# Performance work log

Hardware: AMD Instinct MI355X
Metric: run time of the kernel (lower is better)

## Reference

```python
import jax, jax.numpy as jnp
import numpy as np

HIDDEN = 2048
NUM_HEADS = 16
HEAD_DIM = HIDDEN // NUM_HEADS  # 128
SCALE = HEAD_DIM ** -0.5


def setup_inputs() -> dict:
    key = jax.random.key(0)
    ks = jax.random.split(key, 5)
    B, S = 2, 2048
    init = HIDDEN ** -0.5  # roughly kaiming-uniform scale for Linear weights
    return {
        "hidden_states": jax.random.normal(ks[0], (B, S, HIDDEN), dtype=jnp.float32),
        "Wq": jax.random.normal(ks[1], (HIDDEN, HIDDEN), dtype=jnp.float32) * init,
        "Wk": jax.random.normal(ks[2], (HIDDEN, HIDDEN), dtype=jnp.float32) * init,
        "Wv": jax.random.normal(ks[3], (HIDDEN, HIDDEN), dtype=jnp.float32) * init,
        "Wo": jax.random.normal(ks[4], (HIDDEN, HIDDEN), dtype=jnp.float32) * init,
    }


def reference(hidden_states, Wq, Wk, Wv, Wo):
    B, S, _ = hidden_states.shape
    # Projections (nn.Linear: x @ W.T; weights stored as [out, in])
    q = (hidden_states @ Wq.T).reshape(B, S, NUM_HEADS, HEAD_DIM).transpose(0, 2, 1, 3)
    k = (hidden_states @ Wk.T).reshape(B, S, NUM_HEADS, HEAD_DIM).transpose(0, 2, 1, 3)
    v = (hidden_states @ Wv.T).reshape(B, S, NUM_HEADS, HEAD_DIM).transpose(0, 2, 1, 3)
    # Full quadratic attention (faithful to the source's explicit materialization)
    scores = jnp.einsum("bhqd,bhkd->bhqk", q, k) * SCALE  # [B,H,S,S]
    probs = jax.nn.softmax(scores, axis=-1)
    attn = jnp.einsum("bhqk,bhkd->bhqd", probs, v)  # [B,H,S,Dh]
    attn = attn.transpose(0, 2, 1, 3).reshape(B, S, HIDDEN)
    return attn @ Wo.T
```

## Files before the change

kernel.cpp:

```cpp
#include <hip/hip_runtime.h>
#include <cstdint>

#define HIDDEN 2048
#define NHEADS 16
#define DH 128
#define BATCH 2
#define SEQ 2048
#define MTOT 4096
#define BH (BATCH * NHEADS)

typedef __attribute__((ext_vector_type(8))) short bf16x8;
typedef __attribute__((ext_vector_type(4))) float f32x4;

static constexpr float QSCALE = (float)(0.08838834764831845 * 1.4426950408889634);

__device__ __forceinline__ unsigned short f2bf(float f) {
  union { float f; uint32_t u; } v; v.f = f;
  uint32_t r = v.u + 0x7FFFu + ((v.u >> 16) & 1u);
  return (unsigned short)(r >> 16);
}
__device__ __forceinline__ uint32_t cvtpk(float lo, float hi) {
  uint32_t r;
  asm("v_cvt_pk_bf16_f32 %0, %1, %2" : "=v"(r) : "v"(lo), "v"(hi));
  return r;
}
__device__ __forceinline__ f32x4 mfma16(bf16x8 a, bf16x8 b, f32x4 c) {
  return __builtin_amdgcn_mfma_f32_16x16x32_bf16(a, b, c, 0, 0, 0);
}

typedef const __attribute__((address_space(1))) unsigned char* gas1_t;
typedef __attribute__((address_space(3))) unsigned char* las3_t;
__device__ __forceinline__ void gll16(const void* g, void* l) {
  __builtin_amdgcn_global_load_lds((gas1_t)g, (las3_t)l, 16, 0, 0);
}

__global__ __launch_bounds__(256) void cast_bf16_kernel(const float* __restrict__ in,
                                                        unsigned short* __restrict__ out,
                                                        int n) {
  int i = (blockIdx.x * 256 + threadIdx.x) * 4;
  if (i < n) {
    float4 f = *(const float4*)&in[i];
    ushort4 o;
    o.x = f2bf(f.x); o.y = f2bf(f.y); o.z = f2bf(f.z); o.w = f2bf(f.w);
    *(ushort4*)&out[i] = o;
  }
}

__global__ __launch_bounds__(256) void gemm_qkv3(const unsigned short* __restrict__ A,
                                                 const unsigned short* __restrict__ Wq,
                                                 const unsigned short* __restrict__ Wk,
                                                 const unsigned short* __restrict__ Wv,
                                                 unsigned short* __restrict__ Qb,
                                                 unsigned short* __restrict__ Kb,
                                                 unsigned short* __restrict__ Vb) {
  __shared__ __align__(16) unsigned short As[4096];
  __shared__ __align__(16) unsigned short Ws[4096];
  const int tid = threadIdx.x;
  const int lane = tid & 63, wv = tid >> 6;
  const int wr = wv >> 1, wc = wv & 1;
  const int g = lane >> 4, lr = lane & 15;
  const int which = blockIdx.x >> 4;
  const int m0 = blockIdx.y * 128, n0 = (blockIdx.x & 15) * 128;
  const unsigned short* W = (which == 0) ? Wq : (which == 1) ? Wk : Wv;
  const float alpha = (which == 0) ? QSCALE : 1.0f;

  f32x4 acc[4][4];
#pragma unroll
  for (int i = 0; i < 4; ++i)
#pragma unroll
    for (int j = 0; j < 4; ++j) acc[i][j] = (f32x4){0.f, 0.f, 0.f, 0.f};

  const int c0 = tid, c1 = 256 + tid;
  const int row0 = c0 >> 2, kb0 = (c0 & 3) ^ ((row0 >> 1) & 3);
  const int row1 = c1 >> 2, kb1 = (c1 & 3) ^ ((row1 >> 1) & 3);
  const size_t aoff0 = (size_t)(m0 + row0) * HIDDEN + kb0 * 8;
  const size_t aoff1 = (size_t)(m0 + row1) * HIDDEN + kb1 * 8;
  const size_t woff0 = (size_t)(n0 + row0) * HIDDEN + kb0 * 8;
  const size_t woff1 = (size_t)(n0 + row1) * HIDDEN + kb1 * 8;
  const int swz = ((lr >> 1) & 3) * 16;

  for (int k0 = 0; k0 < HIDDEN; k0 += 32) {
    __syncthreads();
    gll16(A + aoff0 + k0, (char*)As + wv * 1024);
    gll16(W + woff0 + k0, (char*)Ws + wv * 1024);
    gll16(A + aoff1 + k0, (char*)As + 4096 + wv * 1024);
    gll16(W + woff1 + k0, (char*)Ws + 4096 + wv * 1024);
    __syncthreads();

    bf16x8 af[4], wf[4];
#pragma unroll
    for (int mi = 0; mi < 4; ++mi) {
      const int row = wr * 64 + mi * 16 + lr;
      af[mi] = *(const bf16x8*)((const char*)As + row * 64 + ((g * 16) ^ swz));
    }
#pragma unroll
    for (int ni = 0; ni < 4; ++ni) {
      const int row = wc * 64 + ni * 16 + lr;
      wf[ni] = *(const bf16x8*)((const char*)Ws + row * 64 + ((g * 16) ^ swz));
    }
#pragma unroll
    for (int mi = 0; mi < 4; ++mi)
#pragma unroll
      for (int ni = 0; ni < 4; ++ni)
        acc[mi][ni] = mfma16(af[mi], wf[ni], acc[mi][ni]);
  }

  unsigned short* C = (which == 0) ? Qb : (which == 1) ? Kb : Vb;
#pragma unroll
  for (int mi = 0; mi < 4; ++mi)
#pragma unroll
    for (int ni = 0; ni < 4; ++ni)
#pragma unroll
      for (int r = 0; r < 4; ++r) {
        const int row = m0 + wr * 64 + mi * 16 + g * 4 + r;
        const int col = n0 + wc * 64 + ni * 16 + lr;
        const unsigned short v = f2bf(acc[mi][ni][r] * alpha);
        const int b = row >> 11, s = row & (SEQ - 1);
        const int h = col >> 7, d = col & (DH - 1);
        const size_t base = (size_t)(b * NHEADS + h) * SEQ * DH;
        if (which == 0)
          C[base + (size_t)s * DH + d] = v;
        else if (which == 1)
          C[base + (size_t)(s >> 5) * 4096 + (d >> 3) * 256 + (s & 31) * 8 + (d & 7)] = v;
        else
          C[base + (size_t)(s >> 3) * 1024 + d * 8 + (s & 7)] = v;
      }
}

__global__ __launch_bounds__(256) void gemm_out(const unsigned short* __restrict__ A,
                                                const unsigned short* __restrict__ W,
                                                float* __restrict__ C) {
  __shared__ __align__(16) unsigned short As[4096];
  __shared__ __align__(16) unsigned short Ws[4096];
  const int tid = threadIdx.x;
  const int lane = tid & 63, wv = tid >> 6;
  const int wr = wv >> 1, wc = wv & 1;
  const int g = lane >> 4, lr = lane & 15;
  const int m0 = blockIdx.y * 128, n0 = blockIdx.x * 128;

  f32x4 acc[4][4];
#pragma unroll
  for (int i = 0; i < 4; ++i)
#pragma unroll
    for (int j = 0; j < 4; ++j) acc[i][j] = (f32x4){0.f, 0.f, 0.f, 0.f};

  const int c0 = tid, c1 = 256 + tid;
  const int row0 = c0 >> 2, kb0 = (c0 & 3) ^ ((row0 >> 1) & 3);
  const int row1 = c1 >> 2, kb1 = (c1 & 3) ^ ((row1 >> 1) & 3);
  const size_t aoff0 = (size_t)(m0 + row0) * HIDDEN + kb0 * 8;
  const size_t aoff1 = (size_t)(m0 + row1) * HIDDEN + kb1 * 8;
  const size_t woff0 = (size_t)(n0 + row0) * HIDDEN + kb0 * 8;
  const size_t woff1 = (size_t)(n0 + row1) * HIDDEN + kb1 * 8;
  const int swz = ((lr >> 1) & 3) * 16;

  for (int k0 = 0; k0 < HIDDEN; k0 += 32) {
    __syncthreads();
    gll16(A + aoff0 + k0, (char*)As + wv * 1024);
    gll16(W + woff0 + k0, (char*)Ws + wv * 1024);
    gll16(A + aoff1 + k0, (char*)As + 4096 + wv * 1024);
    gll16(W + woff1 + k0, (char*)Ws + 4096 + wv * 1024);
    __syncthreads();

    bf16x8 af[4], wf[4];
#pragma unroll
    for (int mi = 0; mi < 4; ++mi) {
      const int row = wr * 64 + mi * 16 + lr;
      af[mi] = *(const bf16x8*)((const char*)As + row * 64 + ((g * 16) ^ swz));
    }
#pragma unroll
    for (int ni = 0; ni < 4; ++ni) {
      const int row = wc * 64 + ni * 16 + lr;
      wf[ni] = *(const bf16x8*)((const char*)Ws + row * 64 + ((g * 16) ^ swz));
    }
#pragma unroll
    for (int mi = 0; mi < 4; ++mi)
#pragma unroll
      for (int ni = 0; ni < 4; ++ni)
        acc[mi][ni] = mfma16(af[mi], wf[ni], acc[mi][ni]);
  }

#pragma unroll
  for (int mi = 0; mi < 4; ++mi)
#pragma unroll
    for (int ni = 0; ni < 4; ++ni)
#pragma unroll
      for (int r = 0; r < 4; ++r) {
        const int row = m0 + wr * 64 + mi * 16 + g * 4 + r;
        const int col = n0 + wc * 64 + ni * 16 + lr;
        C[(size_t)row * HIDDEN + col] = acc[mi][ni][r];
      }
}

__global__ __launch_bounds__(256, 3) void attn_mfma(const unsigned short* __restrict__ Q,
                                                    const unsigned short* __restrict__ K,
                                                    const unsigned short* __restrict__ V,
                                                    unsigned short* __restrict__ Ab) {
  const int bid = blockIdx.x;
  const int bh = bid & 31;
  const int q0 = (bid >> 5) * 128;
  const int tid = threadIdx.x;
  const int wv = tid >> 6, lane = tid & 63;
  const int g = lane >> 4, lr = lane & 15;
  const unsigned short* Qh = Q + (size_t)bh * SEQ * DH;
  const unsigned short* Kh = K + (size_t)bh * SEQ * DH;
  const unsigned short* Vh = V + (size_t)bh * SEQ * DH;

  __shared__ __align__(16) unsigned short Kls[3][4096];
  __shared__ __align__(16) unsigned short Vls[3][4096];
  __shared__ __align__(16) unsigned short Pw[4][16][40];

  bf16x8 qf[2][4];
#pragma unroll
  for (int m = 0; m < 2; ++m)
#pragma unroll
    for (int kb = 0; kb < 4; ++kb)
      qf[m][kb] = *(const bf16x8*)&Qh[(size_t)(q0 + wv * 32 + m * 16 + lr) * DH +
                                      kb * 32 + g * 8];

  f32x4 acc[2][8];
#pragma unroll
  for (int m = 0; m < 2; ++m)
#pragma unroll
    for (int dn = 0; dn < 8; ++dn) acc[m][dn] = (f32x4){0.f, 0.f, 0.f, 0.f};
  float mrun[2] = {-1e30f, -1e30f};
  float lrun[2] = {0.f, 0.f};

#pragma unroll
  for (int tt = 0; tt < 2; ++tt)
#pragma unroll
    for (int j = 0; j < 2; ++j) {
      const int c = j * 256 + tid;
      gll16(Kh + (size_t)tt * 4096 + c * 8, (char*)&Kls[tt][0] + j * 4096 + wv * 1024);
      gll16(Vh + (size_t)tt * 4096 + c * 8, (char*)&Vls[tt][0] + j * 4096 + wv * 1024);
    }

  for (int t = 0; t < 64; ++t) {
    const int cur = t % 3;
    asm volatile("s_waitcnt vmcnt(4)" ::: "memory");
    __builtin_amdgcn_s_barrier();
    if (t + 2 < 64) {
      const int nx = (t + 2) % 3;
      const unsigned short* Kn = Kh + (size_t)(t + 2) * 4096;
      const unsigned short* Vn = Vh + (size_t)(t + 2) * 4096;
      char* kd = (char*)&Kls[nx][0];
      char* vd = (char*)&Vls[nx][0];
#pragma unroll
      for (int j = 0; j < 2; ++j) {
        const int c = j * 256 + tid;
        gll16(Kn + (size_t)c * 8, kd + j * 4096 + wv * 1024);
        gll16(Vn + (size_t)c * 8, vd + j * 4096 + wv * 1024);
      }
    }

    const char* Kc = (const char*)&Kls[cur][0];
    const char* Vc = (const char*)&Vls[cur][0];
    bf16x8 ap[2];
#pragma unroll
    for (int m = 0; m < 2; ++m) {
      f32x4 st0 = (f32x4){0.f, 0.f, 0.f, 0.f};
      f32x4 st1 = (f32x4){0.f, 0.f, 0.f, 0.f};
      __builtin_amdgcn_s_setprio(1);
#pragma unroll
      for (int kb = 0; kb < 4; ++kb) {
        const int cb = (kb * 4 + g) * 32;
        bf16x8 kf0 = *(const bf16x8*)(Kc + (cb + lr) * 16);
        bf16x8 kf1 = *(const bf16x8*)(Kc + (cb + 16 + lr) * 16);
        st0 = mfma16(kf0, qf[m][kb], st0);
        st1 = mfma16(kf1, qf[m][kb], st1);
      }
      __builtin_amdgcn_s_setprio(0);
      float mt = fmaxf(fmaxf(fmaxf(st0[0], st0[1]), fmaxf(st0[2], st0[3])),
                       fmaxf(fmaxf(st1[0], st1[1]), fmaxf(st1[2], st1[3])));
      mt = fmaxf(mt, __shfl_xor(mt, 16));
      mt = fmaxf(mt, __shfl_xor(mt, 32));
      if (!__all(mt <= mrun[m] + 8.0f)) {
        const float mnew = fmaxf(mrun[m], mt);
        const float corr = __builtin_amdgcn_exp2f(mrun[m] - mnew);
        lrun[m] *= corr;
        mrun[m] = mnew;
        const f32x4 cv = (f32x4){__shfl(corr, g * 4 + 0), __shfl(corr, g * 4 + 1),
                                 __shfl(corr, g * 4 + 2), __shfl(corr, g * 4 + 3)};
#pragma unroll
        for (int dn = 0; dn < 8; ++dn) acc[m][dn] *= cv;
      }
      float p[8], ls = 0.f;
#pragma unroll
      for (int r = 0; r < 4; ++r) {
        p[r] = __builtin_amdgcn_exp2f(st0[r] - mrun[m]);
        p[4 + r] = __builtin_amdgcn_exp2f(st1[r] - mrun[m]);
        ls += p[r] + p[4 + r];
      }
      lrun[m] += ls;
      uint2 pk0, pk1;
      pk0.x = cvtpk(p[0], p[1]); pk0.y = cvtpk(p[2], p[3]);
      pk1.x = cvtpk(p[4], p[5]); pk1.y = cvtpk(p[6], p[7]);
      *(uint2*)&Pw[wv][lr][4 * g] = pk0;
      *(uint2*)&Pw[wv][lr][16 + 4 * g] = pk1;
      ap[m] = *(const bf16x8*)&Pw[wv][lr][8 * g];
    }
    __builtin_amdgcn_s_setprio(1);
#pragma unroll
    for (int dn = 0; dn < 8; ++dn) {
      bf16x8 vf = *(const bf16x8*)(Vc + (g * 128 + dn * 16 + lr) * 16);
      acc[0][dn] = mfma16(ap[0], vf, acc[0][dn]);
      acc[1][dn] = mfma16(ap[1], vf, acc[1][dn]);
    }
    __builtin_amdgcn_s_setprio(0);
  }

  const int b = bh >> 4, h = bh & 15;
#pragma unroll
  for (int m = 0; m < 2; ++m) {
    lrun[m] += __shfl_xor(lrun[m], 16);
    lrun[m] += __shfl_xor(lrun[m], 32);
    const float inv = 1.f / lrun[m];
    float ir[4];
#pragma unroll
    for (int r = 0; r < 4; ++r) ir[r] = __shfl(inv, g * 4 + r);
#pragma unroll
    for (int dn = 0; dn < 8; ++dn)
#pragma unroll
      for (int r = 0; r < 4; ++r) {
        const int srow = q0 + wv * 32 + m * 16 + g * 4 + r;
        Ab[((size_t)(b * SEQ + srow) * NHEADS + h) * DH + dn * 16 + lr] =
            f2bf(acc[m][dn][r] * ir[r]);
      }
  }
}

extern "C" void kernel_launch(void* const* d_in, const int* in_sizes, int n_in,
                              void* d_out, int out_size, void* d_ws,
                              size_t ws_size, hipStream_t stream) {
  const float* X  = (const float*)d_in[0];
  const float* Wq = (const float*)d_in[1];
  const float* Wk = (const float*)d_in[2];
  const float* Wv = (const float*)d_in[3];
  const float* Wo = (const float*)d_in[4];
  float* out = (float*)d_out;

  const int n1 = MTOT * HIDDEN;
  const int n2 = HIDDEN * HIDDEN;

  char* p = (char*)d_ws;
  unsigned short* Xb  = (unsigned short*)(p + 0);
  unsigned short* Qb  = (unsigned short*)(p + 16777216);
  unsigned short* Kb  = (unsigned short*)(p + 33554432);
  unsigned short* Vb  = (unsigned short*)(p + 50331648);
  unsigned short* Wqb = (unsigned short*)(p + 67108864);
  unsigned short* Wkb = (unsigned short*)(p + 75497472);
  unsigned short* Wvb = (unsigned short*)(p + 83886080);
  unsigned short* Wob = (unsigned short*)(p + 92274688);
  unsigned short* Ab  = (unsigned short*)(p + 100663296);

  cast_bf16_kernel<<<n1 / 1024, 256, 0, stream>>>(X, Xb, n1);
  cast_bf16_kernel<<<n2 / 1024, 256, 0, stream>>>(Wq, Wqb, n2);
  cast_bf16_kernel<<<n2 / 1024, 256, 0, stream>>>(Wk, Wkb, n2);
  cast_bf16_kernel<<<n2 / 1024, 256, 0, stream>>>(Wv, Wvb, n2);
  cast_bf16_kernel<<<n2 / 1024, 256, 0, stream>>>(Wo, Wob, n2);

  gemm_qkv3<<<dim3(48, MTOT / 128), 256, 0, stream>>>(Xb, Wqb, Wkb, Wvb, Qb, Kb, Vb);

  attn_mfma<<<dim3(512), 256, 0, stream>>>(Qb, Kb, Vb, Ab);

  gemm_out<<<dim3(HIDDEN / 128, MTOT / 128), 256, 0, stream>>>(Ab, Wob, out);
}
```

Before: 304.8 us.

## Pipeline projection GEMMs with 4-stage async LDS ring and 128x256 tiles

Replaces the QKV and output projection GEMMs with 512-thread blocks computing 128x256 tiles. A 4-slot LDS ring buffer is filled by global_load_lds three K-steps ahead, and progress is tracked with explicit vmcnt waits and a single barrier per step. MFMA sections are wrapped in raised wave priority. This aims to hide global load latency and halve the barriers, at the cost of 96KB LDS per block (one block per CU) and fewer blocks in the grid.

Result: faster. 287.6 us (-5.6%).

```diff
diff --git a/kernel.cpp b/kernel.cpp
--- a/kernel.cpp
+++ b/kernel.cpp
@@ -32,6 +32,13 @@
 typedef __attribute__((address_space(3))) unsigned char* las3_t;
 __device__ __forceinline__ void gll16(const void* g, void* l) {
   __builtin_amdgcn_global_load_lds((gas1_t)g, (las3_t)l, 16, 0, 0);
+}
+
+template <int N>
+__device__ __forceinline__ void waitvm() {
+  if constexpr (N == 6) asm volatile("s_waitcnt vmcnt(6)" ::: "memory");
+  else if constexpr (N == 3) asm volatile("s_waitcnt vmcnt(3)" ::: "memory");
+  else asm volatile("s_waitcnt vmcnt(0)" ::: "memory");
 }
 
 __global__ __launch_bounds__(256) void cast_bf16_kernel(const float* __restrict__ in,
@@ -46,65 +53,82 @@
   }
 }
 
-__global__ __launch_bounds__(256) void gemm_qkv3(const unsigned short* __restrict__ A,
-                                                 const unsigned short* __restrict__ Wq,
-                                                 const unsigned short* __restrict__ Wk,
-                                                 const unsigned short* __restrict__ Wv,
-                                                 unsigned short* __restrict__ Qb,
-                                                 unsigned short* __restrict__ Kb,
-                                                 unsigned short* __restrict__ Vb) {
-  __shared__ __align__(16) unsigned short As[4096];
-  __shared__ __align__(16) unsigned short Ws[4096];
+template <int VM>
+__device__ __forceinline__ void gemm_body(int kt, char* SM,
+                                          const unsigned short* pA,
+                                          const unsigned short* pB0,
+                                          const unsigned short* pB1,
+                                          int wv, int wr, int wc, int g, int lr,
+                                          f32x4 (&acc)[4][4]) {
+  waitvm<VM>();
+  __builtin_amdgcn_s_barrier();
+  if (kt + 3 < 64) {
+    char* slot = SM + ((kt + 3) & 3) * 24576;
+    const size_t ko = (size_t)(kt + 3) * 32;
+    gll16(pA + ko, slot + wv * 1024);
+    gll16(pB0 + ko, slot + 8192 + wv * 1024);
+    gll16(pB1 + ko, slot + 16384 + wv * 1024);
+  }
+  const char* Ac = SM + (kt & 3) * 24576;
+  const char* Bc = Ac + 8192;
+  const int fx = (lr >> 1) & 3;
+  bf16x8 af[4], bfr[4];
+#pragma unroll
+  for (int mi = 0; mi < 4; ++mi)
+    af[mi] = *(const bf16x8*)(Ac + (wr * 64 + mi * 16 + lr) * 64 + ((g ^ fx) * 16));
+#pragma unroll
+  for (int ni = 0; ni < 4; ++ni)
+    bfr[ni] = *(const bf16x8*)(Bc + (wc * 64 + ni * 16 + lr) * 64 + ((g ^ fx) * 16));
+  __builtin_amdgcn_s_setprio(1);
+#pragma unroll
+  for (int mi = 0; mi < 4; ++mi)
+#pragma unroll
+    for (int ni = 0; ni < 4; ++ni)
+      acc[mi][ni] = mfma16(af[mi], bfr[ni], acc[mi][ni]);
+  __builtin_amdgcn_s_setprio(0);
+}
+
+__global__ __launch_bounds__(512) void gemm_qkv_pipe(const unsigned short* __restrict__ A,
+                                                     const unsigned short* __restrict__ Wq,
+                                                     const unsigned short* __restrict__ Wk,
+                                                     const unsigned short* __restrict__ Wv,
+                                                     unsigned short* __restrict__ Qb,
+                                                     unsigned short* __restrict__ Kb,
+                                                     unsigned short* __restrict__ Vb) {
+  __shared__ __align__(16) char SM[98304];
   const int tid = threadIdx.x;
   const int lane = tid & 63, wv = tid >> 6;
-  const int wr = wv >> 1, wc = wv & 1;
+  const int wr = wv >> 2, wc = wv & 3;
   const int g = lane >> 4, lr = lane & 15;
-  const int which = blockIdx.x >> 4;
-  const int m0 = blockIdx.y * 128, n0 = (blockIdx.x & 15) * 128;
+  const int which = blockIdx.x >> 3;
+  const int m0 = blockIdx.y * 128, n0 = (blockIdx.x & 7) * 256;
   const unsigned short* W = (which == 0) ? Wq : (which == 1) ? Wk : Wv;
+
+  const int rA = tid >> 2, cA = (tid & 3) ^ ((rA >> 1) & 3);
+  const unsigned short* pA = A + (size_t)(m0 + rA) * HIDDEN + cA * 8;
+  const unsigned short* pB0 = W + (size_t)(n0 + rA) * HIDDEN + cA * 8;
+  const unsigned short* pB1 = W + (size_t)(n0 + 128 + rA) * HIDDEN + cA * 8;
+
+  f32x4 acc[4][4];
+#pragma unroll
+  for (int i = 0; i < 4; ++i)
+#pragma unroll
+    for (int j = 0; j < 4; ++j) acc[i][j] = (f32x4){0.f, 0.f, 0.f, 0.f};
+
+#pragma unroll
+  for (int t = 0; t < 3; ++t) {
+    char* slot = SM + t * 24576;
+    gll16(pA + t * 32, slot + wv * 1024);
+    gll16(pB0 + t * 32, slot + 8192 + wv * 1024);
+    gll16(pB1 + t * 32, slot + 16384 + wv * 1024);
+  }
+
+  for (int kt = 0; kt < 62; ++kt)
+    gemm_body<6>(kt, SM, pA, pB0, pB1, wv, wr, wc, g, lr, acc);
+  gemm_body<3>(62, SM, pA, pB0, pB1, wv, wr, wc, g, lr, acc);
+  gemm_body<0>(63, SM, pA, pB0, pB1, wv, wr, wc, g, lr, acc);
+
   const float alpha = (which == 0) ? QSCALE : 1.0f;
-
-  f32x4 acc[4][4];
-#pragma unroll
-  for (int i = 0; i < 4; ++i)
-#pragma unroll
-    for (int j = 0; j < 4; ++j) acc[i][j] = (f32x4){0.f, 0.f, 0.f, 0.f};
-
-  const int c0 = tid, c1 = 256 + tid;
-  const int row0 = c0 >> 2, kb0 = (c0 & 3) ^ ((row0 >> 1) & 3);
-  const int row1 = c1 >> 2, kb1 = (c1 & 3) ^ ((row1 >> 1) & 3);
-  const size_t aoff0 = (size_t)(m0 + row0) * HIDDEN + kb0 * 8;
-  const size_t aoff1 = (size_t)(m0 + row1) * HIDDEN + kb1 * 8;
-  const size_t woff0 = (size_t)(n0 + row0) * HIDDEN + kb0 * 8;
-  const size_t woff1 = (size_t)(n0 + row1) * HIDDEN + kb1 * 8;
-  const int swz = ((lr >> 1) & 3) * 16;
-
-  for (int k0 = 0; k0 < HIDDEN; k0 += 32) {
-    __syncthreads();
-    gll16(A + aoff0 + k0, (char*)As + wv * 1024);
-    gll16(W + woff0 + k0, (char*)Ws + wv * 1024);
-    gll16(A + aoff1 + k0, (char*)As + 4096 + wv * 1024);
-    gll16(W + woff1 + k0, (char*)Ws + 4096 + wv * 1024);
-    __syncthreads();
-
-    bf16x8 af[4], wf[4];
-#pragma unroll
-    for (int mi = 0; mi < 4; ++mi) {
-      const int row = wr * 64 + mi * 16 + lr;
-      af[mi] = *(const bf16x8*)((const char*)As + row * 64 + ((g * 16) ^ swz));
-    }
-#pragma unroll
-    for (int ni = 0; ni < 4; ++ni) {
-      const int row = wc * 64 + ni * 16 + lr;
-      wf[ni] = *(const bf16x8*)((const char*)Ws + row * 64 + ((g * 16) ^ swz));
-    }
-#pragma unroll
-    for (int mi = 0; mi < 4; ++mi)
-#pragma unroll
-      for (int ni = 0; ni < 4; ++ni)
-        acc[mi][ni] = mfma16(af[mi], wf[ni], acc[mi][ni]);
-  }
-
   unsigned short* C = (which == 0) ? Qb : (which == 1) ? Kb : Vb;
 #pragma unroll
   for (int mi = 0; mi < 4; ++mi)
@@ -127,16 +151,20 @@
       }
 }
 
-__global__ __launch_bounds__(256) void gemm_out(const unsigned short* __restrict__ A,
-                                                const unsigned short* __restrict__ W,
-                                                float* __restrict__ C) {
-  __shared__ __align__(16) unsigned short As[4096];
-  __shared__ __align__(16) unsigned short Ws[4096];
+__global__ __launch_bounds__(512) void gemm_out_pipe(const unsigned short* __restrict__ A,
+                                                     const unsigned short* __restrict__ W,
+                                                     float* __restrict__ C) {
+  __shared__ __align__(16) char SM[98304];
   const int tid = threadIdx.x;
   const int lane = tid & 63, wv = tid >> 6;
-  const int wr = wv >> 1, wc = wv & 1;
+  const int wr = wv >> 2, wc = wv & 3;
   const int g = lane >> 4, lr = lane & 15;
-  const int m0 = blockIdx.y * 128, n0 = blockIdx.x * 128;
+  const int m0 = blockIdx.y * 128, n0 = blockIdx.x * 256;
+
+  const int rA = tid >> 2, cA = (tid & 3) ^ ((rA >> 1) & 3);
+  const unsigned short* pA = A + (size_t)(m0 + rA) * HIDDEN + cA * 8;
+  const unsigned short* pB0 = W + (size_t)(n0 + rA) * HIDDEN + cA * 8;
+  const unsigned short* pB1 = W + (size_t)(n0 + 128 + rA) * HIDDEN + cA * 8;
 
   f32x4 acc[4][4];
 #pragma unroll
@@ -144,40 +172,18 @@
 #pragma unroll
     for (int j = 0; j < 4; ++j) acc[i][j] = (f32x4){0.f, 0.f, 0.f, 0.f};
 
-  const int c0 = tid, c1 = 256 + tid;
-  const int row0 = c0 >> 2, kb0 = (c0 & 3) ^ ((row0 >> 1) & 3);
-  const int row1 = c1 >> 2, kb1 = (c1 & 3) ^ ((row1 >> 1) & 3);
-  const size_t aoff0 = (size_t)(m0 + row0) * HIDDEN + kb0 * 8;
-  const size_t aoff1 = (size_t)(m0 + row1) * HIDDEN + kb1 * 8;
-  const size_t woff0 = (size_t)(n0 + row0) * HIDDEN + kb0 * 8;
-  const size_t woff1 = (size_t)(n0 + row1) * HIDDEN + kb1 * 8;
-  const int swz = ((lr >> 1) & 3) * 16;
-
-  for (int k0 = 0; k0 < HIDDEN; k0 += 32) {
-    __syncthreads();
-    gll16(A + aoff0 + k0, (char*)As + wv * 1024);
-    gll16(W + woff0 + k0, (char*)Ws + wv * 1024);
-    gll16(A + aoff1 + k0, (char*)As + 4096 + wv * 1024);
-    gll16(W + woff1 + k0, (char*)Ws + 4096 + wv * 1024);
-    __syncthreads();
-
-    bf16x8 af[4], wf[4];
-#pragma unroll
-    for (int mi = 0; mi < 4; ++mi) {
-      const int row = wr * 64 + mi * 16 + lr;
-      af[mi] = *(const bf16x8*)((const char*)As + row * 64 + ((g * 16) ^ swz));
-    }
-#pragma unroll
-    for (int ni = 0; ni < 4; ++ni) {
-      const int row = wc * 64 + ni * 16 + lr;
-      wf[ni] = *(const bf16x8*)((const char*)Ws + row * 64 + ((g * 16) ^ swz));
-    }
-#pragma unroll
-    for (int mi = 0; mi < 4; ++mi)
-#pragma unroll
-      for (int ni = 0; ni < 4; ++ni)
-        acc[mi][ni] = mfma16(af[mi], wf[ni], acc[mi][ni]);
-  }
+#pragma unroll
+  for (int t = 0; t < 3; ++t) {
+    char* slot = SM + t * 24576;
+    gll16(pA + t * 32, slot + wv * 1024);
+    gll16(pB0 + t * 32, slot + 8192 + wv * 1024);
+    gll16(pB1 + t * 32, slot + 16384 + wv * 1024);
+  }
+
+  for (int kt = 0; kt < 62; ++kt)
+    gemm_body<6>(kt, SM, pA, pB0, pB1, wv, wr, wc, g, lr, acc);
+  gemm_body<3>(62, SM, pA, pB0, pB1, wv, wr, wc, g, lr, acc);
+  gemm_body<0>(63, SM, pA, pB0, pB1, wv, wr, wc, g, lr, acc);
 
 #pragma unroll
   for (int mi = 0; mi < 4; ++mi)
@@ -358,9 +364,10 @@
   cast_bf16_kernel<<<n2 / 1024, 256, 0, stream>>>(Wv, Wvb, n2);
   cast_bf16_kernel<<<n2 / 1024, 256, 0, stream>>>(Wo, Wob, n2);
 
-  gemm_qkv3<<<dim3(48, MTOT / 128), 256, 0, stream>>>(Xb, Wqb, Wkb, Wvb, Qb, Kb, Vb);
+  gemm_qkv_pipe<<<dim3(24, MTOT / 128), 512, 0, stream>>>(Xb, Wqb, Wkb, Wvb,
+                                                          Qb, Kb, Vb);
 
   attn_mfma<<<dim3(512), 256, 0, stream>>>(Qb, Kb, Vb, Ab);
 
-  gemm_out<<<dim3(HIDDEN / 128, MTOT / 128), 256, 0, stream>>>(Ab, Wob, out);
-}
+  gemm_out_pipe<<<dim3(HIDDEN / 256, MTOT / 128), 512, 0, stream>>>(Ab, Wob, out);
+}
```
